# Optimization experiments

Measured on AMD Instinct MI355X. Metric: run time of the kernel, lower is better.

Reference implementation:

```python
import jax, jax.numpy as jnp
import numpy as np

DECAY = 0.9
THRESHOLD = 1.0


def setup_inputs() -> dict:
    key = jax.random.key(0)
    k1, k2 = jax.random.split(key)
    B, T, I, N = 128, 512, 1024, 1024
    x = jax.random.normal(k1, (B, T, I), dtype=jnp.float32)
    weights = jax.random.uniform(k2, (N, I), dtype=jnp.float32)  # torch.rand init
    return {"x": x, "weights": weights}


def reference(x, weights):
    # x: [B, T, I], weights: [N, I]
    # Hoist the matmul out of the time loop: currents[t] == weights @ x[:, t, :].T
    currents = jnp.einsum("ni,bti->tnb", weights, x)  # [T, N, B]

    def step(mp, i_t):
        mp = DECAY * mp + i_t
        spike_mask = (mp >= THRESHOLD).astype(mp.dtype)
        mp = mp * (1.0 - spike_mask)  # reset fired neurons
        return mp, spike_mask

    mp0 = jnp.zeros((weights.shape[0], x.shape[0]), dtype=x.dtype)  # [N, B]
    _, masks = jax.lax.scan(step, mp0, currents)
    return masks.sum(axis=0)  # spikes: [N, B]
```

## Files before the change

### kernel.cpp

```cpp
#include <hip/hip_runtime.h>
#include <stdint.h>

#define T_DIM 512
#define B_DIM 128
#define I_DIM 1024
#define N_DIM 1024
#define NB (N_DIM * B_DIM)
#define ROWB 4096

#define DECAY 0.9f
#define THRESH 1.0f

typedef _Float16 f16;
typedef _Float16 f16x8 __attribute__((ext_vector_type(8)));
typedef float f32x4 __attribute__((ext_vector_type(4)));

__global__ __launch_bounds__(256) void split_w_kernel(
    const float* __restrict__ W, f16* __restrict__ Ws)
{
    int gid = blockIdx.x * 256 + threadIdx.x;
    int kc  = gid & 127;
    int row = gid >> 7;
    const float* src = W + (size_t)row * I_DIM + kc * 8;
    f16* dst = Ws + (size_t)row * 2048 + kc * 16;
    float v[8];
    *(float4*)&v[0] = *(const float4*)src;
    *(float4*)&v[4] = *(const float4*)(src + 4);
    f16 hi[8], lo[8];
    #pragma unroll
    for (int j = 0; j < 8; ++j) {
        hi[j] = (f16)v[j];
        lo[j] = (f16)(v[j] - (float)hi[j]);
    }
    *(f16x8*)dst       = *(const f16x8*)hi;
    *(f16x8*)(dst + 8) = *(const f16x8*)lo;
}

__global__ __launch_bounds__(256) void split_x_kernel(
    const float* __restrict__ X, f16* __restrict__ Xc, int t0)
{
    int gid = blockIdx.x * 256 + threadIdx.x;
    int kc = gid & 127;
    int b  = (gid >> 7) & 127;
    int tp = gid >> 14;
    const float* src = X + ((size_t)b * T_DIM + (t0 + tp)) * I_DIM + kc * 8;
    f16* dst = Xc + ((size_t)tp * 128 + b) * 2048 + kc * 16;
    float v[8];
    *(float4*)&v[0] = *(const float4*)src;
    *(float4*)&v[4] = *(const float4*)(src + 4);
    f16 hi[8], lo[8];
    #pragma unroll
    for (int j = 0; j < 8; ++j) {
        hi[j] = (f16)v[j];
        lo[j] = (f16)(v[j] - (float)hi[j]);
    }
    *(f16x8*)dst       = *(const f16x8*)hi;
    *(f16x8*)(dst + 8) = *(const f16x8*)lo;
}

__global__ __launch_bounds__(256, 2) void spk_gemm_kernel(
    const uint8_t* __restrict__ Wsb,
    const uint8_t* __restrict__ Xcb,
    float* __restrict__ C, int tc)
{
    __shared__ __align__(16) uint8_t lds[32768];

    const int tid  = threadIdx.x;
    const int wave = tid >> 6, lane = tid & 63;

    const int nwg = gridDim.x;
    const int q = nwg >> 3, r = nwg & 7;
    const int xcd = blockIdx.x & 7, idx = blockIdx.x >> 3;
    const int wg = (xcd < r ? xcd * (q + 1) : r * (q + 1) + (xcd - r) * q) + idx;
    const int n0 = (wg & 7) << 7;
    const int tp = wg >> 3;

    const uint8_t* srcp[8];
    #pragma unroll
    for (int c = 0; c < 8; ++c) {
        int Gall = (wave * 8 + c) * 64 + lane;
        int G  = Gall & 1023;
        int rr = G >> 3, gg = G & 7;
        int xofs = ((gg ^ (rr & 7)) << 4);
        if (Gall < 1024)
            srcp[c] = Wsb + (size_t)(n0 + rr) * ROWB + xofs;
        else
            srcp[c] = Xcb + ((size_t)tp * 128 + rr) * ROWB + xofs;
    }

    const int wr = ((wave >> 1) << 6);
    const int wc = ((wave & 1) << 6);
    const int l15 = lane & 15, kcg = lane >> 4;
    int aoff[4][2], boff[4][2];
    #pragma unroll
    for (int m = 0; m < 4; ++m) {
        int ra = wr + m * 16 + l15;
        int rb = wc + m * 16 + l15;
        #pragma unroll
        for (int hl = 0; hl < 2; ++hl) {
            int g = (kcg << 1) | hl;
            aoff[m][hl] = ra * 128 + ((g ^ (ra & 7)) << 4);
            boff[m][hl] = 16384 + rb * 128 + ((g ^ (rb & 7)) << 4);
        }
    }

    f32x4 acc[4][4];
    #pragma unroll
    for (int m = 0; m < 4; ++m)
        #pragma unroll
        for (int n = 0; n < 4; ++n) acc[m][n] = (f32x4){0.f, 0.f, 0.f, 0.f};

    for (int k0 = 0; k0 < I_DIM; k0 += 32) {
        __syncthreads();
        #pragma unroll
        for (int c = 0; c < 8; ++c) {
            __builtin_amdgcn_global_load_lds(
                (const __attribute__((address_space(1))) uint8_t*)srcp[c],
                (__attribute__((address_space(3))) uint8_t*)&lds[(wave * 8 + c) << 10],
                16, 0, 0);
            srcp[c] += 128;
        }
        __syncthreads();

        f16x8 Ah[4], Al[4], Bh[4], Bl[4];
        #pragma unroll
        for (int m = 0; m < 4; ++m) {
            Ah[m] = *(const f16x8*)&lds[aoff[m][0]];
            Al[m] = *(const f16x8*)&lds[aoff[m][1]];
            Bh[m] = *(const f16x8*)&lds[boff[m][0]];
            Bl[m] = *(const f16x8*)&lds[boff[m][1]];
        }
        #pragma unroll
        for (int m = 0; m < 4; ++m)
            #pragma unroll
            for (int n = 0; n < 4; ++n) {
                acc[m][n] = __builtin_amdgcn_mfma_f32_16x16x32_f16(Ah[m], Bh[n], acc[m][n], 0, 0, 0);
                acc[m][n] = __builtin_amdgcn_mfma_f32_16x16x32_f16(Ah[m], Bl[n], acc[m][n], 0, 0, 0);
                acc[m][n] = __builtin_amdgcn_mfma_f32_16x16x32_f16(Al[m], Bh[n], acc[m][n], 0, 0, 0);
            }
    }

    float* cp = C + (size_t)tp * NB;
    const int rgrp = (lane >> 4) << 2;
    #pragma unroll
    for (int m = 0; m < 4; ++m) {
        int nrow = n0 + wr + m * 16 + rgrp;
        #pragma unroll
        for (int n = 0; n < 4; ++n) {
            int col = wc + n * 16 + l15;
            #pragma unroll
            for (int j = 0; j < 4; ++j)
                cp[(size_t)(nrow + j) * B_DIM + col] = acc[m][n][j];
        }
    }
}

__global__ __launch_bounds__(256) void spk_scan_kernel(
    const float* __restrict__ cur,
    float* __restrict__ mp_state,
    float* __restrict__ out,
    int tc, int first)
{
    const int nb = blockIdx.x * 256 + threadIdx.x;
    float mp, cnt;
    if (first) { mp = 0.0f; cnt = 0.0f; }
    else       { mp = mp_state[nb]; cnt = out[nb]; }

    const float* p = cur + nb;
    #pragma unroll 8
    for (int t = 0; t < tc; ++t) {
        float c = p[(size_t)t * NB];
        mp = __fadd_rn(__fmul_rn(DECAY, mp), c);
        if (mp >= THRESH) { cnt += 1.0f; mp = 0.0f; }
    }
    mp_state[nb] = mp;
    out[nb] = cnt;
}

extern "C" void kernel_launch(void* const* d_in, const int* in_sizes, int n_in,
                              void* d_out, int out_size, void* d_ws, size_t ws_size,
                              hipStream_t stream) {
    const float* x = (const float*)d_in[0];
    const float* w = (const float*)d_in[1];
    float* out = (float*)d_out;

    uint8_t* ws = (uint8_t*)d_ws;
    float* mp = (float*)ws;
    f16*   Wsp = (f16*)(ws + 524288);
    uint8_t* rest = ws + 524288 + 4194304;
    size_t rem = ws_size - 524288 - 4194304;

    int Tc = (int)(rem / (size_t)(128 * ROWB + NB * 4));
    if (Tc > T_DIM) Tc = T_DIM;
    if (Tc < 1) Tc = 1;

    f16*   Xcp = (f16*)rest;
    float* cur = (float*)(rest + (size_t)Tc * 128 * ROWB);

    split_w_kernel<<<(N_DIM * I_DIM / 8) / 256, 256, 0, stream>>>(w, Wsp);

    int first = 1;
    for (int t0 = 0; t0 < T_DIM; ) {
        int tc = T_DIM - t0;
        if (tc > Tc) tc = Tc;

        split_x_kernel<<<tc * 64, 256, 0, stream>>>(x, Xcp, t0);
        spk_gemm_kernel<<<tc * 8, 256, 0, stream>>>(
            (const uint8_t*)Wsp, (const uint8_t*)Xcp, cur, tc);
        spk_scan_kernel<<<NB / 256, 256, 0, stream>>>(cur, mp, out, tc, first);

        first = 0;
        t0 += tc;
    }
}
```

Baseline: 538.5 us.

## Fuse X fp16 split into GEMM with larger tiles and double-buffered LDS

```diff
diff --git a/kernel.cpp b/kernel.cpp
--- a/kernel.cpp
+++ b/kernel.cpp
@@ -36,34 +36,13 @@
     *(f16x8*)(dst + 8) = *(const f16x8*)lo;
 }
 
-__global__ __launch_bounds__(256) void split_x_kernel(
-    const float* __restrict__ X, f16* __restrict__ Xc, int t0)
+__global__ __launch_bounds__(512, 2) void spk_gemm_kernel(
+    const uint8_t* __restrict__ Wsb,
+    const float* __restrict__ X,
+    float* __restrict__ C,
+    int t0, int tc)
 {
-    int gid = blockIdx.x * 256 + threadIdx.x;
-    int kc = gid & 127;
-    int b  = (gid >> 7) & 127;
-    int tp = gid >> 14;
-    const float* src = X + ((size_t)b * T_DIM + (t0 + tp)) * I_DIM + kc * 8;
-    f16* dst = Xc + ((size_t)tp * 128 + b) * 2048 + kc * 16;
-    float v[8];
-    *(float4*)&v[0] = *(const float4*)src;
-    *(float4*)&v[4] = *(const float4*)(src + 4);
-    f16 hi[8], lo[8];
-    #pragma unroll
-    for (int j = 0; j < 8; ++j) {
-        hi[j] = (f16)v[j];
-        lo[j] = (f16)(v[j] - (float)hi[j]);
-    }
-    *(f16x8*)dst       = *(const f16x8*)hi;
-    *(f16x8*)(dst + 8) = *(const f16x8*)lo;
-}
-
-__global__ __launch_bounds__(256, 2) void spk_gemm_kernel(
-    const uint8_t* __restrict__ Wsb,
-    const uint8_t* __restrict__ Xcb,
-    float* __restrict__ C, int tc)
-{
-    __shared__ __align__(16) uint8_t lds[32768];
+    __shared__ __align__(16) uint8_t lds[131072];
 
     const int tid  = threadIdx.x;
     const int wave = tid >> 6, lane = tid & 63;
@@ -72,85 +51,111 @@
     const int q = nwg >> 3, r = nwg & 7;
     const int xcd = blockIdx.x & 7, idx = blockIdx.x >> 3;
     const int wg = (xcd < r ? xcd * (q + 1) : r * (q + 1) + (xcd - r) * q) + idx;
-    const int n0 = (wg & 7) << 7;
-    const int tp = wg >> 3;
+    const int n0    = (wg & 3) << 8;
+    const int tpair = wg >> 2;
+    const int tA    = t0 + tpair * 2;
 
     const uint8_t* srcp[8];
     #pragma unroll
     for (int c = 0; c < 8; ++c) {
-        int Gall = (wave * 8 + c) * 64 + lane;
-        int G  = Gall & 1023;
-        int rr = G >> 3, gg = G & 7;
-        int xofs = ((gg ^ (rr & 7)) << 4);
-        if (Gall < 1024)
-            srcp[c] = Wsb + (size_t)(n0 + rr) * ROWB + xofs;
-        else
-            srcp[c] = Xcb + ((size_t)tp * 128 + rr) * ROWB + xofs;
-    }
-
-    const int wr = ((wave >> 1) << 6);
-    const int wc = ((wave & 1) << 6);
-    const int l15 = lane & 15, kcg = lane >> 4;
-    int aoff[4][2], boff[4][2];
-    #pragma unroll
-    for (int m = 0; m < 4; ++m) {
-        int ra = wr + m * 16 + l15;
-        int rb = wc + m * 16 + l15;
-        #pragma unroll
-        for (int hl = 0; hl < 2; ++hl) {
-            int g = (kcg << 1) | hl;
-            aoff[m][hl] = ra * 128 + ((g ^ (ra & 7)) << 4);
-            boff[m][hl] = 16384 + rb * 128 + ((g ^ (rb & 7)) << 4);
-        }
-    }
-
-    f32x4 acc[4][4];
-    #pragma unroll
-    for (int m = 0; m < 4; ++m)
+        int G = c * 512 + tid;
+        if (c < 4) {
+            int rr = G >> 3, g = G & 7;
+            int gg = g ^ (rr & 7);
+            srcp[c] = Wsb + (size_t)(n0 + rr) * ROWB + gg * 16;
+        } else {
+            int Gb = G - 2048;
+            int rr = Gb >> 3, g = Gb & 7;
+            int gg = g ^ (rr & 7);
+            int brow = rr & 127, tt = tA + (rr >> 7);
+            srcp[c] = (const uint8_t*)X + ((size_t)brow * T_DIM + tt) * (I_DIM * 4) + gg * 16;
+        }
+    }
+
+    const int wr = wave >> 2, wc = wave & 3;
+    const int l15 = lane & 15, kcg = lane >> 4, l7 = l15 & 7;
+
+    const int aBaseH = (wr * 128 + l15) * 128 + ((((kcg << 1) | 0) ^ l7) << 4);
+    const int aBaseL = (wr * 128 + l15) * 128 + ((((kcg << 1) | 1) ^ l7) << 4);
+    const int bBase0 = 32768 + (wc * 64 + l15) * 128 + ((((kcg << 1) | 0) ^ l7) << 4);
+    const int bBase1 = 32768 + (wc * 64 + l15) * 128 + ((((kcg << 1) | 1) ^ l7) << 4);
+
+    f32x4 acc[8][4];
+    #pragma unroll
+    for (int m = 0; m < 8; ++m)
         #pragma unroll
         for (int n = 0; n < 4; ++n) acc[m][n] = (f32x4){0.f, 0.f, 0.f, 0.f};
 
-    for (int k0 = 0; k0 < I_DIM; k0 += 32) {
-        __syncthreads();
-        #pragma unroll
-        for (int c = 0; c < 8; ++c) {
-            __builtin_amdgcn_global_load_lds(
-                (const __attribute__((address_space(1))) uint8_t*)srcp[c],
-                (__attribute__((address_space(3))) uint8_t*)&lds[(wave * 8 + c) << 10],
-                16, 0, 0);
-            srcp[c] += 128;
-        }
-        __syncthreads();
-
-        f16x8 Ah[4], Al[4], Bh[4], Bl[4];
-        #pragma unroll
-        for (int m = 0; m < 4; ++m) {
-            Ah[m] = *(const f16x8*)&lds[aoff[m][0]];
-            Al[m] = *(const f16x8*)&lds[aoff[m][1]];
-            Bh[m] = *(const f16x8*)&lds[boff[m][0]];
-            Bl[m] = *(const f16x8*)&lds[boff[m][1]];
-        }
-        #pragma unroll
-        for (int m = 0; m < 4; ++m)
-            #pragma unroll
-            for (int n = 0; n < 4; ++n) {
-                acc[m][n] = __builtin_amdgcn_mfma_f32_16x16x32_f16(Ah[m], Bh[n], acc[m][n], 0, 0, 0);
-                acc[m][n] = __builtin_amdgcn_mfma_f32_16x16x32_f16(Ah[m], Bl[n], acc[m][n], 0, 0, 0);
-                acc[m][n] = __builtin_amdgcn_mfma_f32_16x16x32_f16(Al[m], Bh[n], acc[m][n], 0, 0, 0);
+    #pragma unroll
+    for (int c = 0; c < 8; ++c)
+        __builtin_amdgcn_global_load_lds(
+            (const __attribute__((address_space(1))) uint8_t*)srcp[c],
+            (__attribute__((address_space(3))) uint8_t*)&lds[c * 8192 + wave * 1024],
+            16, 0, 0);
+
+    for (int kt = 0; kt < 32; ++kt) {
+        const int buf = kt & 1;
+        __builtin_amdgcn_s_barrier();
+        if (kt + 1 < 32) {
+            const int nb = (buf ^ 1) << 16;
+            #pragma unroll
+            for (int c = 0; c < 8; ++c)
+                __builtin_amdgcn_global_load_lds(
+                    (const __attribute__((address_space(1))) uint8_t*)(srcp[c] + (kt + 1) * 128),
+                    (__attribute__((address_space(3))) uint8_t*)&lds[nb + c * 8192 + wave * 1024],
+                    16, 0, 0);
+            asm volatile("s_waitcnt vmcnt(8)" ::: "memory");
+        } else {
+            asm volatile("s_waitcnt vmcnt(0)" ::: "memory");
+        }
+        __builtin_amdgcn_s_barrier();
+        __builtin_amdgcn_sched_barrier(0);
+
+        const uint8_t* bp = &lds[buf << 16];
+
+        f16x8 Ah[8], Al[8];
+        #pragma unroll
+        for (int m = 0; m < 8; ++m) {
+            Ah[m] = *(const f16x8*)&bp[aBaseH + m * 2048];
+            Al[m] = *(const f16x8*)&bp[aBaseL + m * 2048];
+        }
+        #pragma unroll
+        for (int nf = 0; nf < 4; ++nf) {
+            f32x4 b0 = *(const f32x4*)&bp[bBase0 + nf * 2048];
+            f32x4 b1 = *(const f32x4*)&bp[bBase1 + nf * 2048];
+            float bf[8];
+            bf[0] = b0[0]; bf[1] = b0[1]; bf[2] = b0[2]; bf[3] = b0[3];
+            bf[4] = b1[0]; bf[5] = b1[1]; bf[6] = b1[2]; bf[7] = b1[3];
+            f16x8 Bh, Bl;
+            #pragma unroll
+            for (int j = 0; j < 8; ++j) {
+                f16 h = (f16)bf[j];
+                Bh[j] = h;
+                Bl[j] = (f16)(bf[j] - (float)h);
             }
-    }
-
-    float* cp = C + (size_t)tp * NB;
-    const int rgrp = (lane >> 4) << 2;
-    #pragma unroll
-    for (int m = 0; m < 4; ++m) {
-        int nrow = n0 + wr + m * 16 + rgrp;
-        #pragma unroll
-        for (int n = 0; n < 4; ++n) {
-            int col = wc + n * 16 + l15;
+            __builtin_amdgcn_s_setprio(1);
+            #pragma unroll
+            for (int m = 0; m < 8; ++m) {
+                acc[m][nf] = __builtin_amdgcn_mfma_f32_16x16x32_f16(Ah[m], Bh, acc[m][nf], 0, 0, 0);
+                acc[m][nf] = __builtin_amdgcn_mfma_f32_16x16x32_f16(Ah[m], Bl, acc[m][nf], 0, 0, 0);
+                acc[m][nf] = __builtin_amdgcn_mfma_f32_16x16x32_f16(Al[m], Bh, acc[m][nf], 0, 0, 0);
+            }
+            __builtin_amdgcn_s_setprio(0);
+        }
+    }
+
+    const int tsub = wc >> 1, bb = (wc & 1) * 64;
+    float* cp = C + (size_t)(tpair * 2 + tsub) * NB;
+    const int rg = (lane >> 4) << 2;
+    #pragma unroll
+    for (int m = 0; m < 8; ++m) {
+        int nrow = n0 + wr * 128 + m * 16 + rg;
+        #pragma unroll
+        for (int nf = 0; nf < 4; ++nf) {
+            int col = bb + nf * 16 + l15;
             #pragma unroll
             for (int j = 0; j < 4; ++j)
-                cp[(size_t)(nrow + j) * B_DIM + col] = acc[m][n][j];
+                cp[(size_t)(nrow + j) * B_DIM + col] = acc[m][nf][j];
         }
     }
 }
@@ -185,17 +190,17 @@
     float* out = (float*)d_out;
 
     uint8_t* ws = (uint8_t*)d_ws;
-    float* mp = (float*)ws;
+    float* mp  = (float*)ws;
     f16*   Wsp = (f16*)(ws + 524288);
     uint8_t* rest = ws + 524288 + 4194304;
     size_t rem = ws_size - 524288 - 4194304;
 
-    int Tc = (int)(rem / (size_t)(128 * ROWB + NB * 4));
+    int Tc = (int)(rem / (size_t)(NB * 4));
     if (Tc > T_DIM) Tc = T_DIM;
-    if (Tc < 1) Tc = 1;
-
-    f16*   Xcp = (f16*)rest;
-    float* cur = (float*)(rest + (size_t)Tc * 128 * ROWB);
+    Tc &= ~1;
+    if (Tc < 2) Tc = 2;
+
+    float* cur = (float*)rest;
 
     split_w_kernel<<<(N_DIM * I_DIM / 8) / 256, 256, 0, stream>>>(w, Wsp);
 
@@ -204,9 +209,8 @@
         int tc = T_DIM - t0;
         if (tc > Tc) tc = Tc;
 
-        split_x_kernel<<<tc * 64, 256, 0, stream>>>(x, Xcp, t0);
-        spk_gemm_kernel<<<tc * 8, 256, 0, stream>>>(
-            (const uint8_t*)Wsp, (const uint8_t*)Xcp, cur, tc);
+        spk_gemm_kernel<<<(tc / 2) * 4, 512, 0, stream>>>(
+            (const uint8_t*)Wsp, x, cur, t0, tc);
         spk_scan_kernel<<<NB / 256, 256, 0, stream>>>(cur, mp, out, tc, first);
 
         first = 0;
```

New measurement: 503.7 us. -6.4%, faster.

## Enlarge GEMM tile to 256x256 with double-buffered LDS and phased MFMA schedule

Applied to the files above, without the earlier changes.

```diff
diff --git a/kernel.cpp b/kernel.cpp
--- a/kernel.cpp
+++ b/kernel.cpp
@@ -14,6 +14,8 @@
 typedef _Float16 f16;
 typedef _Float16 f16x8 __attribute__((ext_vector_type(8)));
 typedef float f32x4 __attribute__((ext_vector_type(4)));
+
+#define MFMA16 __builtin_amdgcn_mfma_f32_16x16x32_f16
 
 __global__ __launch_bounds__(256) void split_w_kernel(
     const float* __restrict__ W, f16* __restrict__ Ws)
@@ -58,99 +60,137 @@
     *(f16x8*)(dst + 8) = *(const f16x8*)lo;
 }
 
-__global__ __launch_bounds__(256, 2) void spk_gemm_kernel(
+__global__ __launch_bounds__(512, 2) void spk_gemm_kernel(
     const uint8_t* __restrict__ Wsb,
     const uint8_t* __restrict__ Xcb,
     float* __restrict__ C, int tc)
 {
-    __shared__ __align__(16) uint8_t lds[32768];
+    __shared__ __align__(16) uint8_t lds[131072];
 
     const int tid  = threadIdx.x;
     const int wave = tid >> 6, lane = tid & 63;
-
-    const int nwg = gridDim.x;
-    const int q = nwg >> 3, r = nwg & 7;
-    const int xcd = blockIdx.x & 7, idx = blockIdx.x >> 3;
-    const int wg = (xcd < r ? xcd * (q + 1) : r * (q + 1) + (xcd - r) * q) + idx;
-    const int n0 = (wg & 7) << 7;
-    const int tp = wg >> 3;
-
-    const uint8_t* srcp[8];
-    #pragma unroll
-    for (int c = 0; c < 8; ++c) {
-        int Gall = (wave * 8 + c) * 64 + lane;
-        int G  = Gall & 1023;
+    const int wbase16 = wave << 10;
+
+    const int bid = blockIdx.x;
+    const int n0     = ((bid & 7) >> 1) << 8;
+    const int colblk = ((bid >> 3) << 1) | (bid & 1);
+
+    const uint8_t* srcA[4];
+    const uint8_t* srcB[4];
+    #pragma unroll
+    for (int c = 0; c < 4; ++c) {
+        int G = c * 512 + tid;
         int rr = G >> 3, gg = G & 7;
         int xofs = ((gg ^ (rr & 7)) << 4);
-        if (Gall < 1024)
-            srcp[c] = Wsb + (size_t)(n0 + rr) * ROWB + xofs;
-        else
-            srcp[c] = Xcb + ((size_t)tp * 128 + rr) * ROWB + xofs;
-    }
-
-    const int wr = ((wave >> 1) << 6);
-    const int wc = ((wave & 1) << 6);
-    const int l15 = lane & 15, kcg = lane >> 4;
-    int aoff[4][2], boff[4][2];
-    #pragma unroll
-    for (int m = 0; m < 4; ++m) {
-        int ra = wr + m * 16 + l15;
-        int rb = wc + m * 16 + l15;
-        #pragma unroll
-        for (int hl = 0; hl < 2; ++hl) {
-            int g = (kcg << 1) | hl;
-            aoff[m][hl] = ra * 128 + ((g ^ (ra & 7)) << 4);
-            boff[m][hl] = 16384 + rb * 128 + ((g ^ (rb & 7)) << 4);
-        }
-    }
-
-    f32x4 acc[4][4];
-    #pragma unroll
-    for (int m = 0; m < 4; ++m)
+        srcA[c] = Wsb + (size_t)(n0 + rr) * ROWB + xofs;
+        srcB[c] = Xcb + ((size_t)colblk * 256 + rr) * ROWB + xofs;
+    }
+
+    const int wrb = (wave >> 2) << 7;
+    const int wcb = (wave & 3) << 6;
+    const int l15 = lane & 15, kcg = lane >> 4, l7 = l15 & 7;
+    int aoff[8][2], boff[4][2];
+    #pragma unroll
+    for (int m = 0; m < 8; ++m) {
+        int ra = wrb + m * 16 + l15;
+        aoff[m][0] = ra * 128 + ((((kcg << 1) | 0) ^ l7) << 4);
+        aoff[m][1] = ra * 128 + ((((kcg << 1) | 1) ^ l7) << 4);
+    }
+    #pragma unroll
+    for (int nf = 0; nf < 4; ++nf) {
+        int rb = wcb + nf * 16 + l15;
+        boff[nf][0] = 32768 + rb * 128 + ((((kcg << 1) | 0) ^ l7) << 4);
+        boff[nf][1] = 32768 + rb * 128 + ((((kcg << 1) | 1) ^ l7) << 4);
+    }
+
+    f32x4 acc[8][4];
+    #pragma unroll
+    for (int m = 0; m < 8; ++m)
         #pragma unroll
         for (int n = 0; n < 4; ++n) acc[m][n] = (f32x4){0.f, 0.f, 0.f, 0.f};
 
-    for (int k0 = 0; k0 < I_DIM; k0 += 32) {
-        __syncthreads();
+#define STAGE2(KT, C_) do {                                                   \
+    const int qb_ = (((KT) & 1) << 16);                                       \
+    __builtin_amdgcn_global_load_lds(                                         \
+        (const __attribute__((address_space(1))) uint8_t*)(srcA[C_] + (KT) * 128), \
+        (__attribute__((address_space(3))) uint8_t*)&lds[qb_ + (C_) * 8192 + wbase16], \
+        16, 0, 0);                                                            \
+    __builtin_amdgcn_global_load_lds(                                         \
+        (const __attribute__((address_space(1))) uint8_t*)(srcB[C_] + (KT) * 128), \
+        (__attribute__((address_space(3))) uint8_t*)&lds[qb_ + 32768 + (C_) * 8192 + wbase16], \
+        16, 0, 0);                                                            \
+} while (0)
+
+#define PHASE(KT, P, DOSTAGE, DOVM, VMC) do {                                 \
+    if (DOSTAGE) STAGE2((KT) + 1, P);                                         \
+    if (DOVM) {                                                               \
+        asm volatile("s_waitcnt vmcnt(" #VMC ")" ::: "memory");               \
+        __builtin_amdgcn_s_barrier();                                         \
+    }                                                                         \
+    const uint8_t* bp_ = &lds[(((KT) & 1) << 16)];                            \
+    f16x8 Ah0_ = *(const f16x8*)&bp_[aoff[2 * (P)][0]];                       \
+    f16x8 Al0_ = *(const f16x8*)&bp_[aoff[2 * (P)][1]];                       \
+    f16x8 Ah1_ = *(const f16x8*)&bp_[aoff[2 * (P) + 1][0]];                   \
+    f16x8 Al1_ = *(const f16x8*)&bp_[aoff[2 * (P) + 1][1]];                   \
+    if ((P) == 0) {                                                           \
+        _Pragma("unroll")                                                     \
+        for (int nf_ = 0; nf_ < 4; ++nf_) {                                   \
+            Bh[nf_] = *(const f16x8*)&bp_[boff[nf_][0]];                      \
+            Bl[nf_] = *(const f16x8*)&bp_[boff[nf_][1]];                      \
+        }                                                                     \
+    }                                                                         \
+    asm volatile("s_waitcnt lgkmcnt(0)" ::: "memory");                        \
+    __builtin_amdgcn_sched_barrier(0);                                        \
+    __builtin_amdgcn_s_setprio(1);                                            \
+    _Pragma("unroll")                                                         \
+    for (int nf_ = 0; nf_ < 4; ++nf_)                                         \
+        acc[2 * (P)][nf_]     = MFMA16(Ah0_, Bh[nf_], acc[2 * (P)][nf_], 0, 0, 0); \
+    _Pragma("unroll")                                                         \
+    for (int nf_ = 0; nf_ < 4; ++nf_)                                         \
+        acc[2 * (P) + 1][nf_] = MFMA16(Ah1_, Bh[nf_], acc[2 * (P) + 1][nf_], 0, 0, 0); \
+    _Pragma("unroll")                                                         \
+    for (int nf_ = 0; nf_ < 4; ++nf_)                                         \
+        acc[2 * (P)][nf_]     = MFMA16(Ah0_, Bl[nf_], acc[2 * (P)][nf_], 0, 0, 0); \
+    _Pragma("unroll")                                                         \
+    for (int nf_ = 0; nf_ < 4; ++nf_)                                         \
+        acc[2 * (P) + 1][nf_] = MFMA16(Ah1_, Bl[nf_], acc[2 * (P) + 1][nf_], 0, 0, 0); \
+    _Pragma("unroll")                                                         \
+    for (int nf_ = 0; nf_ < 4; ++nf_)                                         \
+        acc[2 * (P)][nf_]     = MFMA16(Al0_, Bh[nf_], acc[2 * (P)][nf_], 0, 0, 0); \
+    _Pragma("unroll")                                                         \
+    for (int nf_ = 0; nf_ < 4; ++nf_)                                         \
+        acc[2 * (P) + 1][nf_] = MFMA16(Al1_, Bh[nf_], acc[2 * (P) + 1][nf_], 0, 0, 0); \
+    __builtin_amdgcn_s_setprio(0);                                            \
+    __builtin_amdgcn_s_barrier();                                             \
+} while (0)
+
+    #pragma unroll
+    for (int c = 0; c < 4; ++c) STAGE2(0, c);
+
+    f16x8 Bh[4], Bl[4];
+    for (int kt = 0; kt < 31; ++kt) {
+        PHASE(kt, 0, 1, 1, 2);
+        PHASE(kt, 1, 1, 0, 0);
+        PHASE(kt, 2, 1, 0, 0);
+        PHASE(kt, 3, 1, 0, 0);
+    }
+    PHASE(31, 0, 0, 1, 0);
+    PHASE(31, 1, 0, 0, 0);
+    PHASE(31, 2, 0, 0, 0);
+    PHASE(31, 3, 0, 0, 0);
+
+    float* cp = C + (size_t)(colblk * 2 + (wcb >> 7)) * NB;
+    const int rg = (lane >> 4) << 2;
+    const int bb = wcb & 127;
+    #pragma unroll
+    for (int m = 0; m < 8; ++m) {
+        int nrow = n0 + wrb + m * 16 + rg;
         #pragma unroll
-        for (int c = 0; c < 8; ++c) {
-            __builtin_amdgcn_global_load_lds(
-                (const __attribute__((address_space(1))) uint8_t*)srcp[c],
-                (__attribute__((address_space(3))) uint8_t*)&lds[(wave * 8 + c) << 10],
-                16, 0, 0);
-            srcp[c] += 128;
-        }
-        __syncthreads();
-
-        f16x8 Ah[4], Al[4], Bh[4], Bl[4];
-        #pragma unroll
-        for (int m = 0; m < 4; ++m) {
-            Ah[m] = *(const f16x8*)&lds[aoff[m][0]];
-            Al[m] = *(const f16x8*)&lds[aoff[m][1]];
-            Bh[m] = *(const f16x8*)&lds[boff[m][0]];
-            Bl[m] = *(const f16x8*)&lds[boff[m][1]];
-        }
-        #pragma unroll
-        for (int m = 0; m < 4; ++m)
-            #pragma unroll
-            for (int n = 0; n < 4; ++n) {
-                acc[m][n] = __builtin_amdgcn_mfma_f32_16x16x32_f16(Ah[m], Bh[n], acc[m][n], 0, 0, 0);
-                acc[m][n] = __builtin_amdgcn_mfma_f32_16x16x32_f16(Ah[m], Bl[n], acc[m][n], 0, 0, 0);
-                acc[m][n] = __builtin_amdgcn_mfma_f32_16x16x32_f16(Al[m], Bh[n], acc[m][n], 0, 0, 0);
-            }
-    }
-
-    float* cp = C + (size_t)tp * NB;
-    const int rgrp = (lane >> 4) << 2;
-    #pragma unroll
-    for (int m = 0; m < 4; ++m) {
-        int nrow = n0 + wr + m * 16 + rgrp;
-        #pragma unroll
-        for (int n = 0; n < 4; ++n) {
-            int col = wc + n * 16 + l15;
+        for (int nf = 0; nf < 4; ++nf) {
+            int col = bb + nf * 16 + l15;
             #pragma unroll
             for (int j = 0; j < 4; ++j)
-                cp[(size_t)(nrow + j) * B_DIM + col] = acc[m][n][j];
+                cp[(size_t)(nrow + j) * B_DIM + col] = acc[m][nf][j];
         }
     }
 }
@@ -185,14 +225,15 @@
     float* out = (float*)d_out;
 
     uint8_t* ws = (uint8_t*)d_ws;
-    float* mp = (float*)ws;
+    float* mp  = (float*)ws;
     f16*   Wsp = (f16*)(ws + 524288);
     uint8_t* rest = ws + 524288 + 4194304;
     size_t rem = ws_size - 524288 - 4194304;
 
     int Tc = (int)(rem / (size_t)(128 * ROWB + NB * 4));
     if (Tc > T_DIM) Tc = T_DIM;
-    if (Tc < 1) Tc = 1;
+    Tc &= ~1;
+    if (Tc < 2) Tc = 2;
 
     f16*   Xcp = (f16*)rest;
     float* cur = (float*)(rest + (size_t)Tc * 128 * ROWB);
@@ -205,7 +246,7 @@
         if (tc > Tc) tc = Tc;
 
         split_x_kernel<<<tc * 64, 256, 0, stream>>>(x, Xcp, t0);
-        spk_gemm_kernel<<<tc * 8, 256, 0, stream>>>(
+        spk_gemm_kernel<<<(tc / 2) * 4, 512, 0, stream>>>(
             (const uint8_t*)Wsp, (const uint8_t*)Xcp, cur, tc);
         spk_scan_kernel<<<NB / 256, 256, 0, stream>>>(cur, mp, out, tc, first);
 
```

Measured after the change: 520.5 us. 3.3% less time.
